# Performance work log

Measured on AMD Instinct MI355X. Metric: run time of the kernel, lower is better.

## Reference

```python
import jax, jax.numpy as jnp
import numpy as np

B, N, RESC, LAT, UNIT = 8, 32, 256.0, 1536, 512
CHS = [64, 64, 128, 256, 512, 512]
HS = [128, 64, 32, 16, 8, 1]


def _align(feat, P):
    # torch F.grid_sample(feat, 2*P.unsqueeze(-2)/RESC - 1, 'bilinear', 'border', align_corners=False).squeeze(-1)
    # feat: [B,C,H,W], P: [B,M,2] (x,y) pixel coords in [0,RESC); returns [B,C,M]
    Bn, C, H, W = feat.shape
    gx = 2.0 * P[..., 0] / RESC - 1.0
    gy = 2.0 * P[..., 1] / RESC - 1.0
    # align_corners=False unnormalize, then border clamp
    x = jnp.clip(((gx + 1.0) * W - 1.0) * 0.5, 0.0, W - 1.0)
    y = jnp.clip(((gy + 1.0) * H - 1.0) * 0.5, 0.0, H - 1.0)
    x0 = jnp.floor(x); y0 = jnp.floor(y)
    wx = (x - x0)[:, None, :]; wy = (y - y0)[:, None, :]
    x0i = x0.astype(jnp.int32); y0i = y0.astype(jnp.int32)
    x1i = jnp.minimum(x0i + 1, W - 1); y1i = jnp.minimum(y0i + 1, H - 1)
    flat = feat.reshape(Bn, C, H * W)
    def gat(yi, xi):
        return jnp.take_along_axis(flat, (yi * W + xi)[:, None, :], axis=2)  # [B,C,M]
    v00 = gat(y0i, x0i); v01 = gat(y0i, x1i); v10 = gat(y1i, x0i); v11 = gat(y1i, x1i)
    return v00 * (1 - wx) * (1 - wy) + v01 * wx * (1 - wy) + v10 * (1 - wx) * wy + v11 * wx * wy


def _conv1(x, w, b):
    # 1x1 Conv1d: [B,Cin,M] x [Cout,Cin] -> [B,Cout,M]
    return jnp.einsum('bci,oc->boi', x, w) + b[None, :, None]


def _rescls(x, p):
    # ResCls(n=1): intro -> (relu(BN) -> chorus, residual) -> outro ; BN in eval mode
    iw, ib, bg, bb, bm, bv, cw, cb, ow, ob = p
    x = _conv1(x, iw, ib)
    d = jax.nn.relu((x - bm[None, :, None]) * (bg / jnp.sqrt(bv + 1e-5))[None, :, None] + bb[None, :, None])
    x = x + _conv1(d, cw, cb)
    return _conv1(x, ow, ob)


def _forward(feats, P, n, gp, pp):
    # node features: concat of per-level aligned features  [B, LAT, N]
    F_ = jnp.concatenate([_align(f, P) for f in feats], axis=1)
    # edge midpoints ep[b, i*N+j] = (P[i] + P[j]) / 2  -> [B, N*N, 2]
    ep = ((P[:, :, None, :] + P[:, None, :, :]) * 0.5).reshape(B, N * N, 2)
    # L: first LAT channels = F[:, :, i], next LAT channels = F[:, :, j]
    Fi = jnp.broadcast_to(F_[:, :, :, None], (B, LAT, N, N)).reshape(B, LAT, N * N)
    Fj = jnp.broadcast_to(F_[:, :, None, :], (B, LAT, N, N)).reshape(B, LAT, N * N)
    E = jnp.concatenate([_align(f, ep) for f in feats], axis=1)  # [B, LAT, N*N]
    CE = jnp.concatenate([Fi, Fj, E], axis=1)  # [B, 3*LAT, N*N]
    gate = jax.nn.sigmoid(_rescls(CE, gp))  # [B, 1, N*N]
    pr = _rescls(CE, pp)  # [B, 64, N*N]
    pr = pr / jnp.maximum(jnp.linalg.norm(pr, axis=1, keepdims=True), 1e-12)  # F.normalize(dim=1)
    m = jnp.arange(N) < n[:, None]  # [B, N]
    mask = (m[:, None, :] & m[:, :, None]).reshape(B, 1, N * N).astype(CE.dtype)
    return (gate * pr * mask).reshape(B, 64, N, N)


def setup_inputs() -> dict:
    key = jax.random.key(0)
    ks = jax.random.split(key, 20)
    d = {}
    for i, (c, h) in enumerate(zip(CHS, HS)):
        d[f'feat{i}'] = jax.random.normal(ks[i], (B, c, h, h), jnp.float32)
    d['P'] = jax.random.uniform(ks[6], (B, N, 2), jnp.float32) * RESC
    d['n'] = jax.random.randint(ks[7], (B,), 16, N + 1, jnp.int32)
    def w(k, shape):
        return jax.random.normal(k, shape, jnp.float32) * 0.02
    for pre, cout, k0 in (('g', 1, 8), ('p', 64, 12)):
        d[pre + '_iw'] = w(ks[k0], (UNIT, 3 * LAT)); d[pre + '_ib'] = jnp.zeros((UNIT,), jnp.float32)
        d[pre + '_bg'] = jnp.ones((UNIT,), jnp.float32); d[pre + '_bb'] = jnp.zeros((UNIT,), jnp.float32)
        d[pre + '_bm'] = jnp.zeros((UNIT,), jnp.float32)
        d[pre + '_bv'] = jax.random.uniform(ks[k0 + 1], (UNIT,), jnp.float32) + 0.5
        d[pre + '_cw'] = w(ks[k0 + 2], (UNIT, UNIT)); d[pre + '_cb'] = jnp.zeros((UNIT,), jnp.float32)
        d[pre + '_ow'] = w(ks[k0 + 3], (cout, UNIT)); d[pre + '_ob'] = jnp.zeros((cout,), jnp.float32)
    return d


def reference(feat0, feat1, feat2, feat3, feat4, feat5, P, n,
              g_iw, g_ib, g_bg, g_bb, g_bm, g_bv, g_cw, g_cb, g_ow, g_ob,
              p_iw, p_ib, p_bg, p_bb, p_bm, p_bv, p_cw, p_cb, p_ow, p_ob):
    feats = (feat0, feat1, feat2, feat3, feat4, feat5)
    gp = (g_iw, g_ib, g_bg, g_bb, g_bm, g_bv, g_cw, g_cb, g_ow, g_ob)
    pp = (p_iw, p_ib, p_bg, p_bb, p_bm, p_bv, p_cw, p_cb, p_ow, p_ob)
    return _forward(feats, P, n, gp, pp)
```

## Files before the change

### kernel.cpp

```cpp
#include <hip/hip_runtime.h>
#include <hip/hip_bf16.h>

using bf16 = __hip_bfloat16;
using short8 = __attribute__((ext_vector_type(8))) short;
using f32x4  = __attribute__((ext_vector_type(4))) float;
typedef unsigned int u32;

#define LAT_ 1536

__device__ __forceinline__ void glds16(const bf16* g, bf16* l) {
  __builtin_amdgcn_global_load_lds(
      (const __attribute__((address_space(1))) void*)g,
      (__attribute__((address_space(3))) void*)l, 16, 0, 0);
}
__device__ __forceinline__ float b2f(bf16 x) { return __bfloat162float(x); }
__device__ __forceinline__ bf16 f2b(float x) { return __float2bfloat16(x); }

template<int C, int W>
__device__ __forceinline__ void trans_tile(const float* __restrict__ src, bf16* __restrict__ dst,
                                           int b, int hw0, int c0, bf16 (*tile)[72], int t) {
  constexpr int HW = W * W;
  {
    int cl = t >> 2, h0 = (t & 3) * 16;
    const float* sp = src + (long)(b * C + c0 + cl) * HW + hw0 + h0;
    #pragma unroll
    for (int k = 0; k < 16; k += 4) {
      float4 v = *(const float4*)(sp + k);
      tile[h0 + k + 0][cl] = f2b(v.x);
      tile[h0 + k + 1][cl] = f2b(v.y);
      tile[h0 + k + 2][cl] = f2b(v.z);
      tile[h0 + k + 3][cl] = f2b(v.w);
    }
  }
  __syncthreads();
  {
    int hwl = t >> 2, cc = (t & 3) * 16;
    bf16* dp = dst + ((long)b * HW + hw0 + hwl) * C + c0 + cc;
    #pragma unroll
    for (int k = 0; k < 16; k += 2) {
      __hip_bfloat162 pr;
      pr.x = tile[hwl][cc + k];
      pr.y = tile[hwl][cc + k + 1];
      *(__hip_bfloat162*)(dp + k) = pr;
    }
  }
}

__global__ __launch_bounds__(256) void prep_k(
    const float* __restrict__ g_iw, const float* __restrict__ p_iw,
    const float* __restrict__ p_cw, const float* __restrict__ p_ow, const float* __restrict__ f5,
    const float* __restrict__ g_bg, const float* __restrict__ g_bb, const float* __restrict__ g_bm,
    const float* __restrict__ g_bv, const float* __restrict__ p_bg, const float* __restrict__ p_bb,
    const float* __restrict__ p_bm, const float* __restrict__ p_bv,
    const float* __restrict__ g_ib, const float* __restrict__ p_ib, const float* __restrict__ p_cb,
    const float* __restrict__ g_ow, const float* __restrict__ g_cw,
    const float* __restrict__ g_cb, const float* __restrict__ g_ob,
    const float* __restrict__ f0, const float* __restrict__ f1, const float* __restrict__ f2,
    const float* __restrict__ f3, const float* __restrict__ f4,
    bf16* __restrict__ Wp, bf16* __restrict__ pcw16, bf16* __restrict__ pow16,
    bf16* __restrict__ T5, float* __restrict__ bnp, float* __restrict__ u,
    float* __restrict__ gacc,
    bf16* __restrict__ T0, bf16* __restrict__ T1, bf16* __restrict__ T2,
    bf16* __restrict__ T3, bf16* __restrict__ T4) {
  __shared__ bf16 tile[64][72];
  __shared__ float red[256];
  int B = blockIdx.x, t = threadIdx.x;
  if (B < 18432) {
    int seg = B / 3072;
    int idx = (B % 3072) * 256 + t;
    if (idx < 512 * 1536) {
      int r = idx / 1536, c = idx % 1536;
      const float* src; int co;
      switch (seg) {
        case 0: src = g_iw; co = 0;    break;
        case 1: src = g_iw; co = 1536; break;
        case 2: src = p_iw; co = 0;    break;
        case 3: src = p_iw; co = 1536; break;
        case 4: src = g_iw; co = 3072; break;
        default: src = p_iw; co = 3072; break;
      }
      Wp[(long)seg * 512 * 1536 + idx] = f2b(src[(long)r * 4608 + co + c]);
    }
    return;
  }
  if (B < 19456) { int idx = (B - 18432) * 256 + t; pcw16[idx] = f2b(p_cw[idx]); return; }
  if (B < 19584) { int idx = (B - 19456) * 256 + t; pow16[idx] = f2b(p_ow[idx]); return; }
  if (B < 19600) { int idx = (B - 19584) * 256 + t; T5[idx] = f2b(f5[idx]); return; }
  if (B < 19602) {
    int k = (B - 19600) * 256 + t;
    if (k < 512) {
      float sg = g_bg[k] / sqrtf(g_bv[k] + 1e-5f);
      bnp[k] = sg; bnp[512 + k] = g_bb[k] - g_bm[k] * sg;
      float sp = p_bg[k] / sqrtf(p_bv[k] + 1e-5f);
      bnp[1024 + k] = sp; bnp[1536 + k] = p_bb[k] - p_bm[k] * sp;
      bnp[2048 + k] = g_ib[k]; bnp[2560 + k] = p_ib[k];
      bnp[3584 + k] = p_cb[k];
    }
    return;
  }
  if (B < 19610) {
    __shared__ float ured[4][64];
    int k0 = (B - 19602) * 64;
    int kk = t & 63, part = t >> 6;
    int k = k0 + kk;
    float s = 0.f;
    for (int o = part * 128; o < part * 128 + 128; ++o)
      s = fmaf(g_ow[o], g_cw[o * 512 + k], s);
    ured[part][kk] = s;
    __syncthreads();
    if (part == 0) u[k] = ured[0][kk] + ured[1][kk] + ured[2][kk] + ured[3][kk];
    return;
  }
  if (B == 19610) {
    red[t] = g_ow[t] * g_cb[t] + g_ow[t + 256] * g_cb[t + 256];
    __syncthreads();
    for (int off = 128; off; off >>= 1) {
      if (t < off) red[t] += red[t + off];
      __syncthreads();
    }
    if (t == 0) bnp[3072] = red[0] + g_ob[0];
    return;
  }
  if (B < 19643) { int idx = (B - 19611) * 256 + t; gacc[idx] = 0.f; return; }
  {
    int q = B - 19643;
    int b = q / 376, tt = q % 376;
    if (tt < 256)      trans_tile<64, 128>(f0, T0, b, tt * 64, 0, tile, t);
    else if (tt < 320) trans_tile<64, 64 >(f1, T1, b, (tt - 256) * 64, 0, tile, t);
    else if (tt < 352) { int z = tt - 320; trans_tile<128, 32>(f2, T2, b, (z & 15) * 64, (z >> 4) * 64, tile, t); }
    else if (tt < 368) { int z = tt - 352; trans_tile<256, 16>(f3, T3, b, (z & 3) * 64, (z >> 2) * 64, tile, t); }
    else               { int z = tt - 368; trans_tile<512, 8 >(f4, T4, b, 0, z * 64, tile, t); }
  }
}

__device__ __forceinline__ float blo(u32 r) { return __uint_as_float(r << 16); }
__device__ __forceinline__ float bhi(u32 r) { return __uint_as_float(r & 0xffff0000u); }

template<int C, int W>
__device__ __forceinline__ void proc2(const bf16* __restrict__ T, int b,
    const float* MX, const float* MY, bf16* __restrict__ Sb, int koff, int t) {
  constexpr int C2 = C / 2, HW = W * W;
  const bf16* Tb = T + (long)b * HW * C;
  for (int idx = t; idx < 16 * C2; idx += 256) {
    int q = idx / C2, c2 = idx % C2;
    float x = MX[q], y = MY[q];
    float fx = fminf(fmaxf(x * ((float)W / 256.f) - 0.5f, 0.f), (float)(W - 1));
    float fy = fminf(fmaxf(y * ((float)W / 256.f) - 0.5f, 0.f), (float)(W - 1));
    float x0f = floorf(fx), y0f = floorf(fy);
    float wx = fx - x0f, wy = fy - y0f;
    int x0 = (int)x0f, y0 = (int)y0f;
    int x1 = min(x0 + 1, W - 1), y1 = min(y0 + 1, W - 1);
    u32 r00 = *(const u32*)&Tb[(y0 * W + x0) * C + 2 * c2];
    u32 r01 = *(const u32*)&Tb[(y0 * W + x1) * C + 2 * c2];
    u32 r10 = *(const u32*)&Tb[(y1 * W + x0) * C + 2 * c2];
    u32 r11 = *(const u32*)&Tb[(y1 * W + x1) * C + 2 * c2];
    float w00 = (1.f - wx) * (1.f - wy), w01 = wx * (1.f - wy);
    float w10 = (1.f - wx) * wy,        w11 = wx * wy;
    float vlo = blo(r00) * w00 + blo(r01) * w01 + blo(r10) * w10 + blo(r11) * w11;
    float vhi = bhi(r00) * w00 + bhi(r01) * w01 + bhi(r10) * w10 + bhi(r11) * w11;
    __hip_bfloat162 pr;
    pr.x = f2b(vlo); pr.y = f2b(vhi);
    *(__hip_bfloat162*)&Sb[(long)q * LAT_ + koff + 2 * c2] = pr;
  }
}

__global__ __launch_bounds__(256) void sample5_k(
    const bf16* __restrict__ T0, const bf16* __restrict__ T1, const bf16* __restrict__ T2,
    const bf16* __restrict__ T3, const bf16* __restrict__ T4, const bf16* __restrict__ T5,
    const float* __restrict__ P, bf16* __restrict__ Sball) {
  int b = blockIdx.z, p0 = blockIdx.x * 16, lvl = blockIdx.y, t = threadIdx.x;
  __shared__ float Px[32], Py[32], MX[16], MY[16];
  if (t < 32) { Px[t] = P[(b * 32 + t) * 2]; Py[t] = P[(b * 32 + t) * 2 + 1]; }
  __syncthreads();
  if (t < 16) {
    int m = p0 + t;
    float x, y;
    if (m < 32) { x = Px[m]; y = Py[m]; }
    else { int ij = m - 32, i = ij >> 5, j = ij & 31;
           x = 0.5f * (Px[i] + Px[j]); y = 0.5f * (Py[i] + Py[j]); }
    MX[t] = x; MY[t] = y;
  }
  __syncthreads();
  bf16* Sb = Sball + ((long)b * 1056 + p0) * LAT_;
  switch (lvl) {
    case 0: proc2<64, 128>(T0, b, MX, MY, Sb, 0,    t); break;
    case 1: proc2<64, 64 >(T1, b, MX, MY, Sb, 64,   t); break;
    case 2: proc2<128, 32>(T2, b, MX, MY, Sb, 128,  t); break;
    case 3: proc2<256, 16>(T3, b, MX, MY, Sb, 256,  t); break;
    case 4: proc2<512, 8 >(T4, b, MX, MY, Sb, 512,  t); break;
    default:
      for (int idx = t; idx < 16 * 256; idx += 256) {
        int q = idx >> 8, c2 = idx & 255;
        *(__hip_bfloat162*)&Sb[(long)q * LAT_ + 1024 + 2 * c2] =
            *(const __hip_bfloat162*)&T5[b * 512 + 2 * c2];
      }
  }
}

__global__ __launch_bounds__(256) void nodegemm_k(
    const bf16* __restrict__ Sball, const bf16* __restrict__ Wp, float* __restrict__ A4) {
  int b = blockIdx.y;
  int n0 = blockIdx.x * 64;
  int t = threadIdx.x, w = t >> 6, lane = t & 63;
  int nn = n0 + w * 16;
  int frow = lane & 15, fko = (lane >> 4) * 8;
  const bf16* Ab = Sball + (long)b * 1056 * LAT_;
  f32x4 acc[2] = {};
  for (int kb = 0; kb < LAT_; kb += 32) {
    short8 bq = *(const short8*)&Wp[(long)(nn + frow) * LAT_ + kb + fko];
    #pragma unroll
    for (int i = 0; i < 2; ++i) {
      short8 aq = *(const short8*)&Ab[(long)(i * 16 + frow) * LAT_ + kb + fko];
      acc[i] = __builtin_amdgcn_mfma_f32_16x16x32_bf16(aq, bq, acc[i], 0, 0, 0);
    }
  }
  #pragma unroll
  for (int i = 0; i < 2; ++i)
    #pragma unroll
    for (int r = 0; r < 4; ++r) {
      int m = i * 16 + (lane >> 4) * 4 + r;
      int n = nn + (lane & 15);
      A4[(long)b * 65536 + m * 2048 + n] = acc[i][r];
    }
}

__global__ __launch_bounds__(256) void edge_k(
    const bf16* __restrict__ Sball, const bf16* __restrict__ WpE,
    const float* __restrict__ bnp, const float* __restrict__ A4,
    const float* __restrict__ u, const float* __restrict__ g_ow,
    bf16* __restrict__ XFh, bf16* __restrict__ DH, float* __restrict__ gacc) {
  int b = blockIdx.z;
  int m0 = blockIdx.x * 128, n0 = blockIdx.y * 128;
  const bf16* A = Sball + (long)b * 1056 * LAT_ + 32 * LAT_;
  __shared__ bf16 Ash[2][128 * 64];
  __shared__ bf16 Bsh[2][128 * 64];
  int t = threadIdx.x, w = t >> 6, lane = t & 63;
  int mh = (w & 1) * 64, nh = (w >> 1) * 64;
  int frow = lane & 15, kq = lane >> 4;
  int srow = w * 8 + (lane >> 3), schunk = lane & 7;
  int rx7 = frow & 7;
  f32x4 acc[4][4] = {};

  auto STAGE = [&](int buf, int kt) {
    int kb = kt * 64;
    #pragma unroll
    for (int q = 0; q < 4; ++q) {
      int ra = q * 32 + srow;
      int sc = (schunk ^ (ra & 7)) * 8;
      glds16(&A[(long)(m0 + ra) * LAT_ + kb + sc],   &Ash[buf][ra * 64 + schunk * 8]);
      glds16(&WpE[(long)(n0 + ra) * LAT_ + kb + sc], &Bsh[buf][ra * 64 + schunk * 8]);
    }
  };

  STAGE(0, 0);
  STAGE(1, 1);
  asm volatile("s_waitcnt vmcnt(8)" ::: "memory");
  __builtin_amdgcn_sched_barrier(0);
  __builtin_amdgcn_s_barrier();
  #pragma unroll 1
  for (int kt = 0; kt < 24; ++kt) {
    int c = kt & 1;
    short8 af[2][4], bq[2][4];
    #pragma unroll
    for (int h = 0; h < 2; ++h) {
      int s8 = (((h * 4 + kq) ^ rx7) << 3);
      #pragma unroll
      for (int i = 0; i < 4; ++i)
        af[h][i] = *(const short8*)&Ash[c][(mh + i * 16 + frow) * 64 + s8];
      #pragma unroll
      for (int j = 0; j < 4; ++j)
        bq[h][j] = *(const short8*)&Bsh[c][(nh + j * 16 + frow) * 64 + s8];
    }
    asm volatile("s_waitcnt lgkmcnt(0)" ::: "memory");
    __builtin_amdgcn_sched_barrier(0);
    __builtin_amdgcn_s_barrier();
    if (kt + 2 < 24) STAGE(c, kt + 2);
    __builtin_amdgcn_sched_barrier(0);
    __builtin_amdgcn_s_setprio(1);
    #pragma unroll
    for (int h = 0; h < 2; ++h)
      #pragma unroll
      for (int i = 0; i < 4; ++i)
        #pragma unroll
        for (int j = 0; j < 4; ++j)
          acc[i][j] = __builtin_amdgcn_mfma_f32_16x16x32_bf16(af[h][i], bq[h][j], acc[i][j], 0, 0, 0);
    __builtin_amdgcn_s_setprio(0);
    if (kt < 23) {
      if (kt + 2 < 24) {
        asm volatile("s_waitcnt vmcnt(8)" ::: "memory");
      } else {
        asm volatile("s_waitcnt vmcnt(0)" ::: "memory");
      }
      __builtin_amdgcn_sched_barrier(0);
      __builtin_amdgcn_s_barrier();
    }
  }
  if (n0 < 512) {
    float pg[16];
    #pragma unroll
    for (int z = 0; z < 16; ++z) pg[z] = 0.f;
    #pragma unroll
    for (int i = 0; i < 4; ++i) {
      #pragma unroll
      for (int j = 0; j < 4; ++j) {
        int n = n0 + nh + j * 16 + (lane & 15);
        float gw = g_ow[n], uu = u[n];
        float sc2 = bnp[n], sh = bnp[512 + n], ib = bnp[2048 + n];
        #pragma unroll
        for (int r = 0; r < 4; ++r) {
          int m = m0 + mh + i * 16 + (lane >> 4) * 4 + r;
          float v = acc[i][j][r] + ib
                  + A4[((long)b * 32 + (m >> 5)) * 2048 + n]
                  + A4[((long)b * 32 + (m & 31)) * 2048 + 512 + n];
          float d = fmaxf(fmaf(v, sc2, sh), 0.f);
          pg[i * 4 + r] += gw * v + uu * d;
        }
      }
    }
    #pragma unroll
    for (int z = 0; z < 16; ++z) {
      float v = pg[z];
      v += __shfl_xor(v, 1, 16);
      v += __shfl_xor(v, 2, 16);
      v += __shfl_xor(v, 4, 16);
      v += __shfl_xor(v, 8, 16);
      pg[z] = v;
    }
    if ((lane & 15) == 0) {
      #pragma unroll
      for (int z = 0; z < 16; ++z) {
        int m = m0 + mh + (z >> 2) * 16 + (lane >> 4) * 4 + (z & 3);
        atomicAdd(&gacc[(long)b * 1024 + m], pg[z]);
      }
    }
  } else {
    #pragma unroll
    for (int i = 0; i < 4; ++i) {
      #pragma unroll
      for (int j = 0; j < 4; ++j) {
        int n = n0 + nh + j * 16 + (lane & 15);
        int np = n - 512;
        float sc2 = bnp[1024 + np], sh = bnp[1536 + np], ib = bnp[2048 + n];
        #pragma unroll
        for (int r = 0; r < 4; ++r) {
          int m = m0 + mh + i * 16 + (lane >> 4) * 4 + r;
          float v = acc[i][j][r] + ib
                  + A4[((long)b * 32 + (m >> 5)) * 2048 + 1024 + np]
                  + A4[((long)b * 32 + (m & 31)) * 2048 + 1536 + np];
          long e = ((long)b * 1024 + m) * 512 + np;
          XFh[e] = f2b(v);
          DH[e]  = f2b(fmaxf(fmaf(v, sc2, sh), 0.f));
        }
      }
    }
  }
}

__global__ __launch_bounds__(256) void chorus_k(
    const bf16* __restrict__ DH, const bf16* __restrict__ pcw16,
    const float* __restrict__ bnp, const bf16* __restrict__ XFh,
    bf16* __restrict__ Yp16) {
  int b = blockIdx.z;
  int m0 = blockIdx.x * 128, n0 = blockIdx.y * 128;
  const bf16* A = DH + (long)b * 1024 * 512;
  __shared__ bf16 Ash[128 * 64];
  __shared__ bf16 Bsh[128 * 64];
  int t = threadIdx.x, w = t >> 6, lane = t & 63;
  int mh = (w & 1) * 64, nh = (w >> 1) * 64;
  int frow = lane & 15, kq = lane >> 4;
  int srow = w * 8 + (lane >> 3), schunk = lane & 7;
  int rx7 = frow & 7;
  f32x4 acc[4][4] = {};
  for (int kb = 0; kb < 512; kb += 64) {
    #pragma unroll
    for (int q = 0; q < 4; ++q) {
      int ra = q * 32 + srow;
      int sc = (schunk ^ (ra & 7)) * 8;
      glds16(&A[(long)(m0 + ra) * 512 + kb + sc],     &Ash[ra * 64 + schunk * 8]);
      glds16(&pcw16[(long)(n0 + ra) * 512 + kb + sc], &Bsh[ra * 64 + schunk * 8]);
    }
    __syncthreads();
    #pragma unroll
    for (int h = 0; h < 2; ++h) {
      int s8 = (((h * 4 + kq) ^ rx7) << 3);
      short8 af[4], bq[4];
      #pragma unroll
      for (int i = 0; i < 4; ++i)
        af[i] = *(const short8*)&Ash[(mh + i * 16 + frow) * 64 + s8];
      #pragma unroll
      for (int j = 0; j < 4; ++j)
        bq[j] = *(const short8*)&Bsh[(nh + j * 16 + frow) * 64 + s8];
      #pragma unroll
      for (int i = 0; i < 4; ++i)
        #pragma unroll
        for (int j = 0; j < 4; ++j)
          acc[i][j] = __builtin_amdgcn_mfma_f32_16x16x32_bf16(af[i], bq[j], acc[i][j], 0, 0, 0);
    }
    __syncthreads();
  }
  #pragma unroll
  for (int i = 0; i < 4; ++i)
    #pragma unroll
    for (int j = 0; j < 4; ++j)
      #pragma unroll
      for (int r = 0; r < 4; ++r) {
        int m = m0 + mh + i * 16 + (lane >> 4) * 4 + r;
        int n = n0 + nh + j * 16 + (lane & 15);
        float v = acc[i][j][r] + bnp[3584 + n]
                + b2f(XFh[((long)b * 1024 + m) * 512 + n]);
        Yp16[((long)b * 1024 + m) * 512 + n] = f2b(v);
      }
}

__global__ __launch_bounds__(256) void ofinal_k(
    const bf16* __restrict__ Yp16, const bf16* __restrict__ pow16,
    const float* __restrict__ p_ob, const float* __restrict__ gacc,
    const float* __restrict__ bnp, const int* __restrict__ nvec,
    float* __restrict__ out) {
  int b = blockIdx.y;
  int m0 = blockIdx.x * 64;
  const bf16* Ab = Yp16 + (long)b * 1024 * 512;
  __shared__ bf16 Ash[64][40];
  __shared__ bf16 Bsh[64][40];
  __shared__ float ol[64][65];
  int t = threadIdx.x, w = t >> 6, lane = t & 63;
  int mq = w * 16;
  int frow = lane & 15, fko = (lane >> 4) * 8;
  f32x4 acc[4] = {};
  for (int kb = 0; kb < 512; kb += 32) {
    { int r = t >> 2, ko = (t & 3) * 8;
      *(uint4*)&Ash[r][ko] = *(const uint4*)&Ab[(long)(m0 + r) * 512 + kb + ko];
      *(uint4*)&Bsh[r][ko] = *(const uint4*)&pow16[(long)r * 512 + kb + ko]; }
    __syncthreads();
    short8 af = *(const short8*)&Ash[mq + frow][fko];
    #pragma unroll
    for (int j = 0; j < 4; ++j) {
      short8 bq = *(const short8*)&Bsh[j * 16 + frow][fko];
      acc[j] = __builtin_amdgcn_mfma_f32_16x16x32_bf16(af, bq, acc[j], 0, 0, 0);
    }
    __syncthreads();
  }
  float pr[4][4], ssl[4] = {0.f, 0.f, 0.f, 0.f};
  #pragma unroll
  for (int j = 0; j < 4; ++j) {
    float bias = p_ob[j * 16 + (lane & 15)];
    #pragma unroll
    for (int r = 0; r < 4; ++r) {
      float v = acc[j][r] + bias;
      pr[j][r] = v;
      ssl[r] = fmaf(v, v, ssl[r]);
    }
  }
  #pragma unroll
  for (int r = 0; r < 4; ++r) {
    float v = ssl[r];
    v += __shfl_xor(v, 1, 16);
    v += __shfl_xor(v, 2, 16);
    v += __shfl_xor(v, 4, 16);
    v += __shfl_xor(v, 8, 16);
    ssl[r] = v;
  }
  int nb = nvec[b];
  float gconst = bnp[3072];
  float scale[4];
  #pragma unroll
  for (int r = 0; r < 4; ++r) {
    int m = m0 + mq + (lane >> 4) * 4 + r;
    float gl = gacc[(long)b * 1024 + m] + gconst;
    float gate = 1.f / (1.f + expf(-gl));
    int ii = m >> 5, jj = m & 31;
    float maskv = (ii < nb && jj < nb) ? 1.f : 0.f;
    scale[r] = gate * maskv / fmaxf(sqrtf(ssl[r]), 1e-12f);
  }
  #pragma unroll
  for (int j = 0; j < 4; ++j)
    #pragma unroll
    for (int r = 0; r < 4; ++r)
      ol[mq + (lane >> 4) * 4 + r][j * 16 + (lane & 15)] = pr[j][r] * scale[r];
  __syncthreads();
  {
    int c = t >> 2, ms = (t & 3) * 16;
    float* op = out + ((long)b * 64 + c) * 1024 + m0 + ms;
    #pragma unroll
    for (int k = 0; k < 16; k += 4) {
      float4 v;
      v.x = ol[ms + k + 0][c];
      v.y = ol[ms + k + 1][c];
      v.z = ol[ms + k + 2][c];
      v.w = ol[ms + k + 3][c];
      *(float4*)(op + k) = v;
    }
  }
}

extern "C" void kernel_launch(void* const* d_in, const int* in_sizes, int n_in,
                              void* d_out, int out_size, void* d_ws, size_t ws_size,
                              hipStream_t stream) {
  const float* f0 = (const float*)d_in[0];
  const float* f1 = (const float*)d_in[1];
  const float* f2 = (const float*)d_in[2];
  const float* f3 = (const float*)d_in[3];
  const float* f4 = (const float*)d_in[4];
  const float* f5 = (const float*)d_in[5];
  const float* P  = (const float*)d_in[6];
  const int*   n  = (const int*)d_in[7];
  const float *g_iw=(const float*)d_in[8],  *g_ib=(const float*)d_in[9],
              *g_bg=(const float*)d_in[10], *g_bb=(const float*)d_in[11],
              *g_bm=(const float*)d_in[12], *g_bv=(const float*)d_in[13],
              *g_cw=(const float*)d_in[14], *g_cb=(const float*)d_in[15],
              *g_ow=(const float*)d_in[16], *g_ob=(const float*)d_in[17];
  const float *p_iw=(const float*)d_in[18], *p_ib=(const float*)d_in[19],
              *p_bg=(const float*)d_in[20], *p_bb=(const float*)d_in[21],
              *p_bm=(const float*)d_in[22], *p_bv=(const float*)d_in[23],
              *p_cw=(const float*)d_in[24], *p_cb=(const float*)d_in[25],
              *p_ow=(const float*)d_in[26], *p_ob=(const float*)d_in[27];
  float* out = (float*)d_out;
  char* wsb = (char*)d_ws;

  bf16*  Sb    = (bf16*)(wsb + 0);
  bf16*  Wp    = (bf16*)(wsb + 25952256);
  bf16*  pcw16 = (bf16*)(wsb + 35389440);
  bf16*  pow16 = (bf16*)(wsb + 35913728);
  bf16*  T5    = (bf16*)(wsb + 35979264);
  float* bnp   = (float*)(wsb + 35987456);
  float* u     = (float*)(wsb + 36003840);
  float* gacc  = (float*)(wsb + 36005888);
  float* A4    = (float*)(wsb + 36038656);
  bf16*  XFh   = (bf16*)(wsb + 38135808);
  bf16*  DH    = (bf16*)(wsb + 46524416);
  bf16*  Yp16  = (bf16*)(wsb + 54913024);
  bf16*  T0 = (bf16*)(wsb + 38135808);
  bf16*  T1 = (bf16*)(wsb + 54913024);
  bf16*  T2 = (bf16*)(wsb + 59107328);
  bf16*  T3 = (bf16*)(wsb + 61204480);
  bf16*  T4 = (bf16*)(wsb + 62253056);
  bf16*  WpE = Wp + (long)2048 * LAT_;

  prep_k<<<22651, 256, 0, stream>>>(g_iw, p_iw, p_cw, p_ow, f5,
      g_bg, g_bb, g_bm, g_bv, p_bg, p_bb, p_bm, p_bv, g_ib, p_ib, p_cb,
      g_ow, g_cw, g_cb, g_ob, f0, f1, f2, f3, f4,
      Wp, pcw16, pow16, T5, bnp, u, gacc, T0, T1, T2, T3, T4);
  sample5_k<<<dim3(66, 6, 8), 256, 0, stream>>>(T0, T1, T2, T3, T4, T5, P, Sb);
  nodegemm_k<<<dim3(32, 8), 256, 0, stream>>>(Sb, Wp, A4);
  edge_k<<<dim3(8, 8, 8), 256, 0, stream>>>(Sb, WpE, bnp, A4, u, g_ow, XFh, DH, gacc);
  chorus_k<<<dim3(8, 4, 8), 256, 0, stream>>>(DH, pcw16, bnp, XFh, Yp16);
  ofinal_k<<<dim3(16, 8), 256, 0, stream>>>(Yp16, pow16, p_ob, gacc, bnp, n, out);
}
```

Measured before the change: 248.3 us.

## Double-buffer chorus GEMM and overlap LDS reads with first-half MFMAs

The chorus GEMM kernel moves from a single-buffered LDS loop with two __syncthreads per k-step to a double-buffered pipeline. The next tile is prefetched with global_load_lds and synchronisation uses explicit vmcnt waits and s_barrier, matching the first GEMM. In both GEMM loops the MFMAs for the first k-half are now issued before the lgkmcnt wait and barrier, so LDS fragment reads overlap matrix math. The cost is twice the LDS for chorus, which may reduce occupancy, and subtle ordering assumptions around the explicit waitcnt values.

New measurement: 253.3 us. 2.0% more time.

```diff
diff --git a/kernel.cpp b/kernel.cpp
--- a/kernel.cpp
+++ b/kernel.cpp
@@ -271,6 +271,14 @@
       for (int j = 0; j < 4; ++j)
         bq[h][j] = *(const short8*)&Bsh[c][(nh + j * 16 + frow) * 64 + s8];
     }
+    __builtin_amdgcn_sched_barrier(0);
+    __builtin_amdgcn_s_setprio(1);
+    #pragma unroll
+    for (int i = 0; i < 4; ++i)
+      #pragma unroll
+      for (int j = 0; j < 4; ++j)
+        acc[i][j] = __builtin_amdgcn_mfma_f32_16x16x32_bf16(af[0][i], bq[0][j], acc[i][j], 0, 0, 0);
+    __builtin_amdgcn_s_setprio(0);
     asm volatile("s_waitcnt lgkmcnt(0)" ::: "memory");
     __builtin_amdgcn_sched_barrier(0);
     __builtin_amdgcn_s_barrier();
@@ -278,12 +286,10 @@
     __builtin_amdgcn_sched_barrier(0);
     __builtin_amdgcn_s_setprio(1);
     #pragma unroll
-    for (int h = 0; h < 2; ++h)
-      #pragma unroll
-      for (int i = 0; i < 4; ++i)
-        #pragma unroll
-        for (int j = 0; j < 4; ++j)
-          acc[i][j] = __builtin_amdgcn_mfma_f32_16x16x32_bf16(af[h][i], bq[h][j], acc[i][j], 0, 0, 0);
+    for (int i = 0; i < 4; ++i)
+      #pragma unroll
+      for (int j = 0; j < 4; ++j)
+        acc[i][j] = __builtin_amdgcn_mfma_f32_16x16x32_bf16(af[1][i], bq[1][j], acc[i][j], 0, 0, 0);
     __builtin_amdgcn_s_setprio(0);
     if (kt < 23) {
       if (kt + 2 < 24) {
@@ -363,40 +369,74 @@
   int b = blockIdx.z;
   int m0 = blockIdx.x * 128, n0 = blockIdx.y * 128;
   const bf16* A = DH + (long)b * 1024 * 512;
-  __shared__ bf16 Ash[128 * 64];
-  __shared__ bf16 Bsh[128 * 64];
+  __shared__ bf16 Ash[2][128 * 64];
+  __shared__ bf16 Bsh[2][128 * 64];
   int t = threadIdx.x, w = t >> 6, lane = t & 63;
   int mh = (w & 1) * 64, nh = (w >> 1) * 64;
   int frow = lane & 15, kq = lane >> 4;
   int srow = w * 8 + (lane >> 3), schunk = lane & 7;
   int rx7 = frow & 7;
   f32x4 acc[4][4] = {};
-  for (int kb = 0; kb < 512; kb += 64) {
+
+  auto STAGE = [&](int buf, int kt) {
+    int kb = kt * 64;
     #pragma unroll
     for (int q = 0; q < 4; ++q) {
       int ra = q * 32 + srow;
       int sc = (schunk ^ (ra & 7)) * 8;
-      glds16(&A[(long)(m0 + ra) * 512 + kb + sc],     &Ash[ra * 64 + schunk * 8]);
-      glds16(&pcw16[(long)(n0 + ra) * 512 + kb + sc], &Bsh[ra * 64 + schunk * 8]);
-    }
-    __syncthreads();
+      glds16(&A[(long)(m0 + ra) * 512 + kb + sc],     &Ash[buf][ra * 64 + schunk * 8]);
+      glds16(&pcw16[(long)(n0 + ra) * 512 + kb + sc], &Bsh[buf][ra * 64 + schunk * 8]);
+    }
+  };
+
+  STAGE(0, 0);
+  STAGE(1, 1);
+  asm volatile("s_waitcnt vmcnt(8)" ::: "memory");
+  __builtin_amdgcn_sched_barrier(0);
+  __builtin_amdgcn_s_barrier();
+  #pragma unroll 1
+  for (int kt = 0; kt < 8; ++kt) {
+    int c = kt & 1;
+    short8 af[2][4], bq[2][4];
     #pragma unroll
     for (int h = 0; h < 2; ++h) {
       int s8 = (((h * 4 + kq) ^ rx7) << 3);
-      short8 af[4], bq[4];
       #pragma unroll
       for (int i = 0; i < 4; ++i)
-        af[i] = *(const short8*)&Ash[(mh + i * 16 + frow) * 64 + s8];
+        af[h][i] = *(const short8*)&Ash[c][(mh + i * 16 + frow) * 64 + s8];
       #pragma unroll
       for (int j = 0; j < 4; ++j)
-        bq[j] = *(const short8*)&Bsh[(nh + j * 16 + frow) * 64 + s8];
-      #pragma unroll
-      for (int i = 0; i < 4; ++i)
-        #pragma unroll
-        for (int j = 0; j < 4; ++j)
-          acc[i][j] = __builtin_amdgcn_mfma_f32_16x16x32_bf16(af[i], bq[j], acc[i][j], 0, 0, 0);
-    }
-    __syncthreads();
+        bq[h][j] = *(const short8*)&Bsh[c][(nh + j * 16 + frow) * 64 + s8];
+    }
+    __builtin_amdgcn_sched_barrier(0);
+    __builtin_amdgcn_s_setprio(1);
+    #pragma unroll
+    for (int i = 0; i < 4; ++i)
+      #pragma unroll
+      for (int j = 0; j < 4; ++j)
+        acc[i][j] = __builtin_amdgcn_mfma_f32_16x16x32_bf16(af[0][i], bq[0][j], acc[i][j], 0, 0, 0);
+    __builtin_amdgcn_s_setprio(0);
+    asm volatile("s_waitcnt lgkmcnt(0)" ::: "memory");
+    __builtin_amdgcn_sched_barrier(0);
+    __builtin_amdgcn_s_barrier();
+    if (kt + 2 < 8) STAGE(c, kt + 2);
+    __builtin_amdgcn_sched_barrier(0);
+    __builtin_amdgcn_s_setprio(1);
+    #pragma unroll
+    for (int i = 0; i < 4; ++i)
+      #pragma unroll
+      for (int j = 0; j < 4; ++j)
+        acc[i][j] = __builtin_amdgcn_mfma_f32_16x16x32_bf16(af[1][i], bq[1][j], acc[i][j], 0, 0, 0);
+    __builtin_amdgcn_s_setprio(0);
+    if (kt < 7) {
+      if (kt + 2 < 8) {
+        asm volatile("s_waitcnt vmcnt(8)" ::: "memory");
+      } else {
+        asm volatile("s_waitcnt vmcnt(0)" ::: "memory");
+      }
+      __builtin_amdgcn_sched_barrier(0);
+      __builtin_amdgcn_s_barrier();
+    }
   }
   #pragma unroll
   for (int i = 0; i < 4; ++i)
```

## Split-K node GEMM with atomics and halve tiles in chorus and output kernels

Applied to the files above, without the earlier changes.

The node GEMM is split along K into four chunks per block and partial sums are accumulated into A4 with atomicAdd. A4 is zeroed by extra blocks appended to the prep kernel. The chorus and final output kernels use smaller M tiles (64 and 32 rows), doubling their grids. The final kernel adds a cross-wave shared-memory reduction for the row norm. The aim is more blocks to fill the GPU's compute units on small grids, at the cost of atomic traffic, extra zeroing, and less operand reuse per block.

Result: faster. 242.7 us (-2.3%).

```diff
diff --git a/kernel.cpp b/kernel.cpp
--- a/kernel.cpp
+++ b/kernel.cpp
@@ -59,7 +59,7 @@
     const float* __restrict__ f3, const float* __restrict__ f4,
     bf16* __restrict__ Wp, bf16* __restrict__ pcw16, bf16* __restrict__ pow16,
     bf16* __restrict__ T5, float* __restrict__ bnp, float* __restrict__ u,
-    float* __restrict__ gacc,
+    float* __restrict__ gacc, float* __restrict__ A4,
     bf16* __restrict__ T0, bf16* __restrict__ T1, bf16* __restrict__ T2,
     bf16* __restrict__ T3, bf16* __restrict__ T4) {
   __shared__ bf16 tile[64][72];
@@ -122,6 +122,7 @@
     return;
   }
   if (B < 19643) { int idx = (B - 19611) * 256 + t; gacc[idx] = 0.f; return; }
+  if (B >= 22651) { int idx = (B - 22651) * 256 + t; A4[idx] = 0.f; return; }
   {
     int q = B - 19643;
     int b = q / 376, tt = q % 376;
@@ -199,14 +200,15 @@
 
 __global__ __launch_bounds__(256) void nodegemm_k(
     const bf16* __restrict__ Sball, const bf16* __restrict__ Wp, float* __restrict__ A4) {
-  int b = blockIdx.y;
+  int b = blockIdx.z;
   int n0 = blockIdx.x * 64;
+  int k0 = blockIdx.y * 384;
   int t = threadIdx.x, w = t >> 6, lane = t & 63;
   int nn = n0 + w * 16;
   int frow = lane & 15, fko = (lane >> 4) * 8;
   const bf16* Ab = Sball + (long)b * 1056 * LAT_;
   f32x4 acc[2] = {};
-  for (int kb = 0; kb < LAT_; kb += 32) {
+  for (int kb = k0; kb < k0 + 384; kb += 32) {
     short8 bq = *(const short8*)&Wp[(long)(nn + frow) * LAT_ + kb + fko];
     #pragma unroll
     for (int i = 0; i < 2; ++i) {
@@ -220,7 +222,7 @@
     for (int r = 0; r < 4; ++r) {
       int m = i * 16 + (lane >> 4) * 4 + r;
       int n = nn + (lane & 15);
-      A4[(long)b * 65536 + m * 2048 + n] = acc[i][r];
+      atomicAdd(&A4[(long)b * 65536 + m * 2048 + n], acc[i][r]);
     }
 }
 
@@ -361,39 +363,44 @@
     const float* __restrict__ bnp, const bf16* __restrict__ XFh,
     bf16* __restrict__ Yp16) {
   int b = blockIdx.z;
-  int m0 = blockIdx.x * 128, n0 = blockIdx.y * 128;
+  int m0 = blockIdx.x * 64, n0 = blockIdx.y * 128;
   const bf16* A = DH + (long)b * 1024 * 512;
-  __shared__ bf16 Ash[128 * 64];
+  __shared__ bf16 Ash[64 * 64];
   __shared__ bf16 Bsh[128 * 64];
   int t = threadIdx.x, w = t >> 6, lane = t & 63;
-  int mh = (w & 1) * 64, nh = (w >> 1) * 64;
+  int nh = w * 32;
   int frow = lane & 15, kq = lane >> 4;
-  int srow = w * 8 + (lane >> 3), schunk = lane & 7;
+  int srow = t >> 3, schunk = t & 7;
   int rx7 = frow & 7;
-  f32x4 acc[4][4] = {};
+  f32x4 acc[4][2] = {};
   for (int kb = 0; kb < 512; kb += 64) {
+    #pragma unroll
+    for (int q = 0; q < 2; ++q) {
+      int ra = q * 32 + srow;
+      int sc = (schunk ^ (ra & 7)) * 8;
+      glds16(&A[(long)(m0 + ra) * 512 + kb + sc], &Ash[ra * 64 + schunk * 8]);
+    }
     #pragma unroll
     for (int q = 0; q < 4; ++q) {
       int ra = q * 32 + srow;
       int sc = (schunk ^ (ra & 7)) * 8;
-      glds16(&A[(long)(m0 + ra) * 512 + kb + sc],     &Ash[ra * 64 + schunk * 8]);
       glds16(&pcw16[(long)(n0 + ra) * 512 + kb + sc], &Bsh[ra * 64 + schunk * 8]);
     }
     __syncthreads();
     #pragma unroll
     for (int h = 0; h < 2; ++h) {
       int s8 = (((h * 4 + kq) ^ rx7) << 3);
-      short8 af[4], bq[4];
+      short8 af[4], bq[2];
       #pragma unroll
       for (int i = 0; i < 4; ++i)
-        af[i] = *(const short8*)&Ash[(mh + i * 16 + frow) * 64 + s8];
-      #pragma unroll
-      for (int j = 0; j < 4; ++j)
+        af[i] = *(const short8*)&Ash[(i * 16 + frow) * 64 + s8];
+      #pragma unroll
+      for (int j = 0; j < 2; ++j)
         bq[j] = *(const short8*)&Bsh[(nh + j * 16 + frow) * 64 + s8];
       #pragma unroll
       for (int i = 0; i < 4; ++i)
         #pragma unroll
-        for (int j = 0; j < 4; ++j)
+        for (int j = 0; j < 2; ++j)
           acc[i][j] = __builtin_amdgcn_mfma_f32_16x16x32_bf16(af[i], bq[j], acc[i][j], 0, 0, 0);
     }
     __syncthreads();
@@ -401,10 +408,10 @@
   #pragma unroll
   for (int i = 0; i < 4; ++i)
     #pragma unroll
-    for (int j = 0; j < 4; ++j)
+    for (int j = 0; j < 2; ++j)
       #pragma unroll
       for (int r = 0; r < 4; ++r) {
-        int m = m0 + mh + i * 16 + (lane >> 4) * 4 + r;
+        int m = m0 + i * 16 + (lane >> 4) * 4 + r;
         int n = n0 + nh + j * 16 + (lane & 15);
         float v = acc[i][j][r] + bnp[3584 + n]
                 + b2f(XFh[((long)b * 1024 + m) * 512 + n]);
@@ -418,32 +425,35 @@
     const float* __restrict__ bnp, const int* __restrict__ nvec,
     float* __restrict__ out) {
   int b = blockIdx.y;
-  int m0 = blockIdx.x * 64;
+  int m0 = blockIdx.x * 32;
   const bf16* Ab = Yp16 + (long)b * 1024 * 512;
-  __shared__ bf16 Ash[64][40];
+  __shared__ bf16 Ash[32][40];
   __shared__ bf16 Bsh[64][40];
-  __shared__ float ol[64][65];
+  __shared__ float sred[2][2][16];
+  __shared__ float ol[32][65];
   int t = threadIdx.x, w = t >> 6, lane = t & 63;
-  int mq = w * 16;
+  int rowg = w & 1, colh = w >> 1;
+  int mq = rowg * 16, cq = colh * 32;
   int frow = lane & 15, fko = (lane >> 4) * 8;
-  f32x4 acc[4] = {};
+  f32x4 acc[2] = {};
   for (int kb = 0; kb < 512; kb += 32) {
-    { int r = t >> 2, ko = (t & 3) * 8;
-      *(uint4*)&Ash[r][ko] = *(const uint4*)&Ab[(long)(m0 + r) * 512 + kb + ko];
-      *(uint4*)&Bsh[r][ko] = *(const uint4*)&pow16[(long)r * 512 + kb + ko]; }
+    { int r = t >> 3, ko = (t & 7) * 4;
+      *(uint2*)&Ash[r][ko] = *(const uint2*)&Ab[(long)(m0 + r) * 512 + kb + ko];
+      int r2 = t >> 2, ko2 = (t & 3) * 8;
+      *(uint4*)&Bsh[r2][ko2] = *(const uint4*)&pow16[(long)r2 * 512 + kb + ko2]; }
     __syncthreads();
     short8 af = *(const short8*)&Ash[mq + frow][fko];
     #pragma unroll
-    for (int j = 0; j < 4; ++j) {
-      short8 bq = *(const short8*)&Bsh[j * 16 + frow][fko];
+    for (int j = 0; j < 2; ++j) {
+      short8 bq = *(const short8*)&Bsh[cq + j * 16 + frow][fko];
       acc[j] = __builtin_amdgcn_mfma_f32_16x16x32_bf16(af, bq, acc[j], 0, 0, 0);
     }
     __syncthreads();
   }
-  float pr[4][4], ssl[4] = {0.f, 0.f, 0.f, 0.f};
+  float pr[2][4], ssl[4] = {0.f, 0.f, 0.f, 0.f};
   #pragma unroll
-  for (int j = 0; j < 4; ++j) {
-    float bias = p_ob[j * 16 + (lane & 15)];
+  for (int j = 0; j < 2; ++j) {
+    float bias = p_ob[cq + j * 16 + (lane & 15)];
     #pragma unroll
     for (int r = 0; r < 4; ++r) {
       float v = acc[j][r] + bias;
@@ -460,29 +470,37 @@
     v += __shfl_xor(v, 8, 16);
     ssl[r] = v;
   }
+  if ((lane & 15) == 0) {
+    #pragma unroll
+    for (int r = 0; r < 4; ++r)
+      sred[rowg][colh][(lane >> 4) * 4 + r] = ssl[r];
+  }
+  __syncthreads();
   int nb = nvec[b];
   float gconst = bnp[3072];
   float scale[4];
   #pragma unroll
   for (int r = 0; r < 4; ++r) {
-    int m = m0 + mq + (lane >> 4) * 4 + r;
+    int row16 = (lane >> 4) * 4 + r;
+    int m = m0 + mq + row16;
+    float s2 = sred[rowg][0][row16] + sred[rowg][1][row16];
     float gl = gacc[(long)b * 1024 + m] + gconst;
     float gate = 1.f / (1.f + expf(-gl));
     int ii = m >> 5, jj = m & 31;
     float maskv = (ii < nb && jj < nb) ? 1.f : 0.f;
-    scale[r] = gate * maskv / fmaxf(sqrtf(ssl[r]), 1e-12f);
+    scale[r] = gate * maskv / fmaxf(sqrtf(s2), 1e-12f);
   }
   #pragma unroll
-  for (int j = 0; j < 4; ++j)
+  for (int j = 0; j < 2; ++j)
     #pragma unroll
     for (int r = 0; r < 4; ++r)
-      ol[mq + (lane >> 4) * 4 + r][j * 16 + (lane & 15)] = pr[j][r] * scale[r];
+      ol[mq + (lane >> 4) * 4 + r][cq + j * 16 + (lane & 15)] = pr[j][r] * scale[r];
   __syncthreads();
   {
-    int c = t >> 2, ms = (t & 3) * 16;
+    int c = t >> 2, ms = (t & 3) * 8;
     float* op = out + ((long)b * 64 + c) * 1024 + m0 + ms;
     #pragma unroll
-    for (int k = 0; k < 16; k += 4) {
+    for (int k = 0; k < 8; k += 4) {
       float4 v;
       v.x = ol[ms + k + 0][c];
       v.y = ol[ms + k + 1][c];
@@ -536,13 +554,13 @@
   bf16*  T4 = (bf16*)(wsb + 62253056);
   bf16*  WpE = Wp + (long)2048 * LAT_;
 
-  prep_k<<<22651, 256, 0, stream>>>(g_iw, p_iw, p_cw, p_ow, f5,
+  prep_k<<<24699, 256, 0, stream>>>(g_iw, p_iw, p_cw, p_ow, f5,
       g_bg, g_bb, g_bm, g_bv, p_bg, p_bb, p_bm, p_bv, g_ib, p_ib, p_cb,
       g_ow, g_cw, g_cb, g_ob, f0, f1, f2, f3, f4,
-      Wp, pcw16, pow16, T5, bnp, u, gacc, T0, T1, T2, T3, T4);
+      Wp, pcw16, pow16, T5, bnp, u, gacc, A4, T0, T1, T2, T3, T4);
   sample5_k<<<dim3(66, 6, 8), 256, 0, stream>>>(T0, T1, T2, T3, T4, T5, P, Sb);
-  nodegemm_k<<<dim3(32, 8), 256, 0, stream>>>(Sb, Wp, A4);
+  nodegemm_k<<<dim3(32, 4, 8), 256, 0, stream>>>(Sb, Wp, A4);
   edge_k<<<dim3(8, 8, 8), 256, 0, stream>>>(Sb, WpE, bnp, A4, u, g_ow, XFh, DH, gacc);
-  chorus_k<<<dim3(8, 4, 8), 256, 0, stream>>>(DH, pcw16, bnp, XFh, Yp16);
-  ofinal_k<<<dim3(16, 8), 256, 0, stream>>>(Yp16, pow16, p_ob, gacc, bnp, n, out);
-}
+  chorus_k<<<dim3(16, 4, 8), 256, 0, stream>>>(DH, pcw16, bnp, XFh, Yp16);
+  ofinal_k<<<dim3(32, 8), 256, 0, stream>>>(Yp16, pow16, p_ob, gacc, bnp, n, out);
+}
```
